# Kernel optimization log

Measured on AMD Instinct MI355X. Metric: run time of the kernel, lower is better.

The kernel has to match this reference:

```python
import jax, jax.numpy as jnp
import numpy as np

# ---- Haar DWT (levels=1, mode='zero'), matches pytorch_wavelets ordering ----
# For even H,W and filter length 2, zero-pad haar analysis reduces to
# non-overlapping 2x2 blocks. Subband order after the two 1D analyses
# (width first, then height): LL, (w-lo,h-hi), (w-hi,h-lo), HH.

def haar_dwt(x):
    a = x[..., 0::2, 0::2]
    b = x[..., 0::2, 1::2]
    c = x[..., 1::2, 0::2]
    d = x[..., 1::2, 1::2]
    ll = (a + b + c + d) * 0.5
    h0 = (a + b - c - d) * 0.5   # lo-width, hi-height
    h1 = (a - b + c - d) * 0.5   # hi-width, lo-height
    hh = (a - b - c + d) * 0.5
    return ll, jnp.stack([h0, h1, hh], axis=2)  # yh: (b,c,3,h/2,w/2)


def _interleave(u, v, axis):
    # interleave two equal-shaped arrays along `axis` (negative axis)
    s = list(u.shape)
    s[axis] *= 2
    return jnp.stack([u, v], axis=axis + len(u.shape) + 1).reshape(s)


def haar_idwt(ll, yh):
    h0, h1, hh = yh[:, :, 0], yh[:, :, 1], yh[:, :, 2]
    a = (ll + h0 + h1 + hh) * 0.5
    b = (ll + h0 - h1 - hh) * 0.5
    c = (ll - h0 + h1 - hh) * 0.5
    d = (ll - h0 - h1 + hh) * 0.5
    top = _interleave(a, b, -1)   # even rows
    bot = _interleave(c, d, -1)   # odd rows
    return _interleave(top, bot, -2)


def batched_dynamic_conv(feat, kernels, pad):
    """feat: (b,cin,h,w), kernels: (b,cout,cin,kh,kw) -> (b,cout,h,w).
    Per-sample kernels via grouped conv (batch as groups)."""
    bsz, cin, h, w = feat.shape
    cout, kh, kw = kernels.shape[1], kernels.shape[3], kernels.shape[4]
    lhs = feat.reshape(1, bsz * cin, h, w)
    rhs = kernels.reshape(bsz * cout, cin, kh, kw)
    out = jax.lax.conv_general_dilated(
        lhs, rhs, window_strides=(1, 1), padding=[(pad, pad), (pad, pad)],
        dimension_numbers=('NCHW', 'OIHW', 'NCHW'), feature_group_count=bsz)
    return out.reshape(bsz, cout, h, w)


def _dyn_conv_subband(feat, sub_kernels, attn_w, attn_b, pad=1):
    # attention: 1x1 conv -> global avg pool -> softmax over kernel_num
    logits = jnp.einsum('bchw,kc->bk', feat, attn_w) / (feat.shape[-2] * feat.shape[-1]) + attn_b
    att = jax.nn.softmax(logits, axis=1)                       # (b,K)
    kernels = jnp.einsum('bk,koiuv->boiuv', att, sub_kernels)  # (b,cout,cin,kh,kw)
    return batched_dynamic_conv(feat, kernels, pad)


def setup_inputs() -> dict:
    key = jax.random.key(0)
    k1, k2, k3, k4 = jax.random.split(key, 4)
    B, C, H, W = 8, 64, 128, 128
    K, SUB, COUT, KS = 4, 4, 64, 3  # kernel_num, 1+3*levels, out_channels, kernel_size
    return {
        'x': jax.random.normal(k1, (B, C, H, W), dtype=jnp.float32),
        'wt_kernels': jax.random.normal(k2, (K, SUB, COUT, C, KS, KS), dtype=jnp.float32) * 0.02,
        'attn_w': jax.random.normal(k3, (K, C), dtype=jnp.float32) * 0.1,
        'attn_b': jnp.zeros((K,), dtype=jnp.float32),
    }


def reference(x, wt_kernels, attn_w, attn_b):
    ll, yh = haar_dwt(x)
    subbands = [ll, yh[:, :, 0], yh[:, :, 1], yh[:, :, 2]]
    outs = [_dyn_conv_subband(sb, wt_kernels[:, i], attn_w, attn_b, pad=1)
            for i, sb in enumerate(subbands)]
    rec_yh = jnp.stack(outs[1:4], axis=2)  # (b,cout,3,h/2,w/2)
    return haar_idwt(outs[0], rec_yh)
```

## Files before the change

kernel.cpp:

```cpp
#include <hip/hip_runtime.h>
#include <hip/hip_bf16.h>
#include <math.h>


typedef __bf16 bf16x8 __attribute__((ext_vector_type(8)));
typedef float f32x4 __attribute__((ext_vector_type(4)));

__device__ __forceinline__ bf16x8 as_bf16x8(uint4 u) {
    union { uint4 a; bf16x8 b; } c; c.a = u; return c.b;
}
__device__ __forceinline__ unsigned short bf16bits(float f) {
    __hip_bfloat16 h = __float2bfloat16(f);
    union { __hip_bfloat16 h; unsigned short u; } c; c.h = h; return c.u;
}
__device__ __forceinline__ void gload_lds16(const uint4* g, uint4* l) {
    __builtin_amdgcn_global_load_lds(
        (const __attribute__((address_space(1))) unsigned int*)g,
        (__attribute__((address_space(3))) unsigned int*)l, 16, 0, 0);
}

#define FPLANE 34848
#define FROW   528

__global__ __launch_bounds__(256)
void dwt_kernel(const float* __restrict__ x, const float* __restrict__ attn_w,
                unsigned short* __restrict__ feats, float* __restrict__ plog) {
    __shared__ uint4 sT[2304];
    __shared__ float sred[64][4];
    unsigned short* sTu = (unsigned short*)sT;
    int y = blockIdx.x, b = blockIdx.y;
    int t = threadIdx.x;
    int c = t >> 2, q = t & 3;

    const float4* r0 = (const float4*)x + ((size_t)(b * 64 + c) * 128 + 2 * y) * 32;
    const float4* r1 = r0 + 32;

    float s0 = 0.f, s1 = 0.f, s2 = 0.f, s3 = 0.f;
    #pragma unroll
    for (int i = 0; i < 8; ++i) {
        int f = i * 4 + q;
        float4 p = r0[f], qq = r1[f];
        int xo = 2 * f;
        {
            float a = p.x, bb = p.y, cc = qq.x, dd = qq.y;
            float ll = (a + bb + cc + dd) * 0.5f, h0 = (a + bb - cc - dd) * 0.5f;
            float h1 = (a - bb + cc - dd) * 0.5f, hh = (a - bb - cc + dd) * 0.5f;
            s0 += ll; s1 += h0; s2 += h1; s3 += hh;
            sTu[0 * 4608 + xo * 72 + c] = bf16bits(ll);
            sTu[1 * 4608 + xo * 72 + c] = bf16bits(h0);
            sTu[2 * 4608 + xo * 72 + c] = bf16bits(h1);
            sTu[3 * 4608 + xo * 72 + c] = bf16bits(hh);
        }
        {
            float a = p.z, bb = p.w, cc = qq.z, dd = qq.w;
            float ll = (a + bb + cc + dd) * 0.5f, h0 = (a + bb - cc - dd) * 0.5f;
            float h1 = (a - bb + cc - dd) * 0.5f, hh = (a - bb - cc + dd) * 0.5f;
            s0 += ll; s1 += h0; s2 += h1; s3 += hh;
            sTu[0 * 4608 + (xo + 1) * 72 + c] = bf16bits(ll);
            sTu[1 * 4608 + (xo + 1) * 72 + c] = bf16bits(h0);
            sTu[2 * 4608 + (xo + 1) * 72 + c] = bf16bits(h1);
            sTu[3 * 4608 + (xo + 1) * 72 + c] = bf16bits(hh);
        }
    }
    s0 += __shfl_xor(s0, 1); s0 += __shfl_xor(s0, 2);
    s1 += __shfl_xor(s1, 1); s1 += __shfl_xor(s1, 2);
    s2 += __shfl_xor(s2, 1); s2 += __shfl_xor(s2, 2);
    s3 += __shfl_xor(s3, 1); s3 += __shfl_xor(s3, 2);
    if (q == 0) { sred[c][0] = s0; sred[c][1] = s1; sred[c][2] = s2; sred[c][3] = s3; }
    __syncthreads();
    if (t < 16) {
        int sub = t >> 2, k = t & 3;
        float acc = 0.f;
        #pragma unroll 8
        for (int cc = 0; cc < 64; ++cc)
            acc += attn_w[k * 64 + cc] * sred[cc][sub];
        plog[((size_t)(b * 4 + sub) * 4 + k) * 64 + y] = acc;
    }
    uint4* fpad = (uint4*)feats;
    const uint4 zz = make_uint4(0u, 0u, 0u, 0u);
    for (int e = t; e < 2112; e += 256) {
        int s = e / 528, r = e - s * 528;
        int px = r >> 3, ck = r & 7;
        uint4 v = zz;
        if (px >= 1 && px <= 64) v = sT[s * 576 + (px - 1) * 9 + ck];
        fpad[((size_t)(b * 4 + s) * 66 + (y + 1)) * FROW + r] = v;
    }
    if (y == 0) {
        for (int e = t; e < 2112; e += 256) {
            int s = e / 528, r = e - s * 528;
            fpad[(size_t)(b * 4 + s) * 66 * FROW + r] = zz;
        }
    } else if (y == 63) {
        for (int e = t; e < 2112; e += 256) {
            int s = e / 528, r = e - s * 528;
            fpad[((size_t)(b * 4 + s) * 66 + 65) * FROW + r] = zz;
        }
    }
}

__global__ __launch_bounds__(256)
void mix_kernel(const float* __restrict__ wt, const float* __restrict__ attn_b,
                const float* __restrict__ plog, unsigned short* __restrict__ wmix) {
    __shared__ float sLw[4][576];
    __shared__ float satt[8][4];
    int co = blockIdx.x, sub = blockIdx.y;
    int t = threadIdx.x;

    if (t < 32) {
        int b = t >> 2, k = t & 3;
        const float* pp = plog + ((size_t)(b * 4 + sub) * 4 + k) * 64;
        float acc = 0.f;
        #pragma unroll 8
        for (int yy = 0; yy < 64; ++yy) acc += pp[yy];
        float logit = acc * (1.0f / 4096.0f) + attn_b[k];
        float m = fmaxf(logit, __shfl_xor(logit, 1));
        m = fmaxf(m, __shfl_xor(m, 2));
        float e = expf(logit - m);
        float s = e + __shfl_xor(e, 1);
        s += __shfl_xor(s, 2);
        satt[b][k] = e / s;
    }
    for (int e = t; e < 2304; e += 256) {
        int k = e / 576, r = e - k * 576;
        sLw[k][r] = wt[((size_t)(k * 4 + sub) * 64 + co) * 576 + r];
    }
    __syncthreads();
    #pragma unroll
    for (int j = 0; j < 18; ++j) {
        int idx = j * 256 + t;
        int b = idx / 576;
        int r = idx - b * 576;
        int tap = r >> 6, ci = r & 63;
        int wi = ci * 9 + tap;
        float v = satt[b][0] * sLw[0][wi] + satt[b][1] * sLw[1][wi]
                + satt[b][2] * sLw[2][wi] + satt[b][3] * sLw[3][wi];
        wmix[((size_t)(b * 4 + sub) * 9 + tap) * 4096 + co * 64 + ci] = bf16bits(v);
    }
}

__device__ __forceinline__ void stage_phase(const uint4* __restrict__ fp,
                                            const uint4* __restrict__ wch,
                                            uint4* sAb, uint4* sWb,
                                            int y0, int x0, int cg, int ck8, int t) {
    #pragma unroll
    for (int i = 0; i < 3; ++i) {
        int e = t + i * 256;
        int py = e / 72, rr = e - py * 72, px = rr >> 2, g = rr & 3;
        gload_lds16(fp + (size_t)((y0 + py) * 66 + x0 + px) * 8 + ck8 + g, &sAb[e]);
    }
    #pragma unroll
    for (int i = 0; i < 4; ++i) {
        int e = t + i * 256;
        int tap = e >> 7, rr = e & 127, co = rr >> 2, g = rr & 3;
        gload_lds16(wch + tap * 512 + (cg * 32 + co) * 8 + ck8 + g, &sWb[e]);
    }
    if (t < 128) {
        int e = 1024 + t;
        int tap = e >> 7, rr = e & 127, co = rr >> 2, g = rr & 3;
        gload_lds16(wch + tap * 512 + (cg * 32 + co) * 8 + ck8 + g, &sWb[e]);
    }
}

__global__ __launch_bounds__(256, 2)
void conv_idwt_kernel(const unsigned short* __restrict__ feats,
                      const unsigned short* __restrict__ wmix,
                      float* __restrict__ out) {
    __shared__ uint4 sA[2][768];
    __shared__ uint4 sW[2][1152];
    int lin = blockIdx.x;
    int b = lin & 7;
    int rest = lin >> 3;
    int cg = rest >> 5, tile = rest & 31;
    int y0 = (tile >> 2) * 8, x0 = (tile & 3) * 16;
    int t = threadIdx.x, w = t >> 6, l = t & 63;
    int l16 = l & 15, kg = l >> 4;
    int wy4 = (w >> 1) * 4, wn = w & 1;

    const uint4* fpb = (const uint4*)feats + (size_t)b * 4 * FPLANE;
    const uint4* wcb = (const uint4*)wmix + (size_t)b * 4 * 4608;

    f32x4 accQ[4][4];
    f32x4 accS[4];
    #pragma unroll
    for (int qd = 0; qd < 4; ++qd)
        #pragma unroll
        for (int r = 0; r < 4; ++r)
            accQ[qd][r] = (f32x4){0.f, 0.f, 0.f, 0.f};
    #pragma unroll
    for (int r = 0; r < 4; ++r) accS[r] = (f32x4){0.f, 0.f, 0.f, 0.f};

    stage_phase(fpb, wcb, sA[0], sW[0], y0, x0, cg, 0, t);
    __syncthreads();

    #pragma unroll
    for (int p = 0; p < 8; ++p) {
        const int sub = p >> 1;
        if (p < 7) {
            const int ns = (p + 1) >> 1, nc = ((p + 1) & 1) * 4;
            stage_phase(fpb + (size_t)ns * FPLANE, wcb + (size_t)ns * 4608,
                        sA[(p + 1) & 1], sW[(p + 1) & 1], y0, x0, cg, nc, t);
        }
        {
            const uint4* A = sA[p & 1];
            const uint4* W = sW[p & 1];
            uint4 af[4][3];
            #pragma unroll
            for (int i = 0; i < 4; ++i)
                #pragma unroll
                for (int dx = 0; dx < 3; ++dx)
                    af[i][dx] = A[((wy4 + i) * 18 + l16 + dx) * 4 + kg];
            __builtin_amdgcn_s_setprio(1);
            #pragma unroll
            for (int dy = 0; dy < 3; ++dy) {
                if (dy > 0) {
                    #pragma unroll
                    for (int i = 0; i < 3; ++i)
                        #pragma unroll
                        for (int dx = 0; dx < 3; ++dx)
                            af[i][dx] = af[i + 1][dx];
                    #pragma unroll
                    for (int dx = 0; dx < 3; ++dx)
                        af[3][dx] = A[((wy4 + dy + 3) * 18 + l16 + dx) * 4 + kg];
                }
                #pragma unroll
                for (int dx = 0; dx < 3; ++dx) {
                    int tap = dy * 3 + dx;
                    bf16x8 bw = as_bf16x8(W[tap * 128 + (wn * 16 + l16) * 4 + kg]);
                    #pragma unroll
                    for (int r = 0; r < 4; ++r)
                        accS[r] = __builtin_amdgcn_mfma_f32_16x16x32_bf16(
                            as_bf16x8(af[r][dx]), bw, accS[r], 0, 0, 0);
                }
            }
            __builtin_amdgcn_s_setprio(0);
        }
        if (p & 1) {
            const float g1 = (sub <= 1) ? 1.f : -1.f;
            const float g2 = (sub == 0 || sub == 2) ? 1.f : -1.f;
            const float g3 = (sub == 0 || sub == 3) ? 1.f : -1.f;
            #pragma unroll
            for (int r = 0; r < 4; ++r) {
                #pragma unroll
                for (int j = 0; j < 4; ++j) {
                    float v = accS[r][j];
                    accQ[0][r][j] += v;
                    accQ[1][r][j] += g1 * v;
                    accQ[2][r][j] += g2 * v;
                    accQ[3][r][j] += g3 * v;
                    accS[r][j] = 0.f;
                }
            }
        }
        __syncthreads();
    }

    #pragma unroll
    for (int r = 0; r < 4; ++r) {
        int y = y0 + wy4 + r;
        int co = cg * 32 + wn * 16 + l16;
        float* otop = out + ((size_t)(b * 64 + co) * 128 + 2 * y) * 128
                          + 2 * (x0 + kg * 4);
        float* obot = otop + 128;
        #pragma unroll
        for (int jp = 0; jp < 2; ++jp) {
            float4 vt, vb;
            vt.x = 0.5f * accQ[0][r][2 * jp];
            vt.y = 0.5f * accQ[1][r][2 * jp];
            vt.z = 0.5f * accQ[0][r][2 * jp + 1];
            vt.w = 0.5f * accQ[1][r][2 * jp + 1];
            vb.x = 0.5f * accQ[2][r][2 * jp];
            vb.y = 0.5f * accQ[3][r][2 * jp];
            vb.z = 0.5f * accQ[2][r][2 * jp + 1];
            vb.w = 0.5f * accQ[3][r][2 * jp + 1];
            *(float4*)(otop + 4 * jp) = vt;
            *(float4*)(obot + 4 * jp) = vb;
        }
    }
}

extern "C" void kernel_launch(void* const* d_in, const int* in_sizes, int n_in,
                              void* d_out, int out_size, void* d_ws, size_t ws_size,
                              hipStream_t stream) {
    const float* x  = (const float*)d_in[0];
    const float* wt = (const float*)d_in[1];
    const float* aw = (const float*)d_in[2];
    const float* ab = (const float*)d_in[3];
    float* out = (float*)d_out;
    char* ws = (char*)d_ws;

    float* plog           = (float*)ws;
    unsigned short* feats = (unsigned short*)(ws + 32768);
    unsigned short* wmix  = (unsigned short*)(ws + 32768 + 17842176);

    hipLaunchKernelGGL(dwt_kernel, dim3(64, 8), dim3(256), 0, stream, x, aw, feats, plog);
    hipLaunchKernelGGL(mix_kernel, dim3(64, 4), dim3(256), 0, stream, wt, ab, plog, wmix);
    hipLaunchKernelGGL(conv_idwt_kernel, dim3(512), dim3(256), 0, stream,
                       feats, wmix, out);
}
```

Before: 117.0 us.

## Fuse DWT, kernel mixing and conv into one persistent kernel with grid barriers

Merges the three launches (DWT, attention/kernel mix, conv+IDWT) into one 512-block kernel that uses software grid barriers built on global atomics, plus a tiny init kernel that resets the barrier counters. The first feature tile is prefetched before the mix phase, so the load overlaps the weight mixing. This removes launch gaps and tail effects between stages. In exchange it depends on all 512 blocks being co-resident (2 per CU) or it can deadlock, and it adds atomic spin-wait overhead.

```diff
diff --git a/kernel.cpp b/kernel.cpp
--- a/kernel.cpp
+++ b/kernel.cpp
@@ -22,162 +22,194 @@
 #define FPLANE 34848
 #define FROW   528
 
-__global__ __launch_bounds__(256)
-void dwt_kernel(const float* __restrict__ x, const float* __restrict__ attn_w,
-                unsigned short* __restrict__ feats, float* __restrict__ plog) {
-    __shared__ uint4 sT[2304];
-    __shared__ float sred[64][4];
-    unsigned short* sTu = (unsigned short*)sT;
-    int y = blockIdx.x, b = blockIdx.y;
-    int t = threadIdx.x;
-    int c = t >> 2, q = t & 3;
-
-    const float4* r0 = (const float4*)x + ((size_t)(b * 64 + c) * 128 + 2 * y) * 32;
-    const float4* r1 = r0 + 32;
-
-    float s0 = 0.f, s1 = 0.f, s2 = 0.f, s3 = 0.f;
-    #pragma unroll
-    for (int i = 0; i < 8; ++i) {
-        int f = i * 4 + q;
-        float4 p = r0[f], qq = r1[f];
-        int xo = 2 * f;
-        {
-            float a = p.x, bb = p.y, cc = qq.x, dd = qq.y;
-            float ll = (a + bb + cc + dd) * 0.5f, h0 = (a + bb - cc - dd) * 0.5f;
-            float h1 = (a - bb + cc - dd) * 0.5f, hh = (a - bb - cc + dd) * 0.5f;
-            s0 += ll; s1 += h0; s2 += h1; s3 += hh;
-            sTu[0 * 4608 + xo * 72 + c] = bf16bits(ll);
-            sTu[1 * 4608 + xo * 72 + c] = bf16bits(h0);
-            sTu[2 * 4608 + xo * 72 + c] = bf16bits(h1);
-            sTu[3 * 4608 + xo * 72 + c] = bf16bits(hh);
-        }
-        {
-            float a = p.z, bb = p.w, cc = qq.z, dd = qq.w;
-            float ll = (a + bb + cc + dd) * 0.5f, h0 = (a + bb - cc - dd) * 0.5f;
-            float h1 = (a - bb + cc - dd) * 0.5f, hh = (a - bb - cc + dd) * 0.5f;
-            s0 += ll; s1 += h0; s2 += h1; s3 += hh;
-            sTu[0 * 4608 + (xo + 1) * 72 + c] = bf16bits(ll);
-            sTu[1 * 4608 + (xo + 1) * 72 + c] = bf16bits(h0);
-            sTu[2 * 4608 + (xo + 1) * 72 + c] = bf16bits(h1);
-            sTu[3 * 4608 + (xo + 1) * 72 + c] = bf16bits(hh);
-        }
-    }
-    s0 += __shfl_xor(s0, 1); s0 += __shfl_xor(s0, 2);
-    s1 += __shfl_xor(s1, 1); s1 += __shfl_xor(s1, 2);
-    s2 += __shfl_xor(s2, 1); s2 += __shfl_xor(s2, 2);
-    s3 += __shfl_xor(s3, 1); s3 += __shfl_xor(s3, 2);
-    if (q == 0) { sred[c][0] = s0; sred[c][1] = s1; sred[c][2] = s2; sred[c][3] = s3; }
+__device__ __forceinline__ void gbar(unsigned* ctr, unsigned* rel,
+                                     unsigned target, unsigned gen) {
     __syncthreads();
-    if (t < 16) {
-        int sub = t >> 2, k = t & 3;
-        float acc = 0.f;
-        #pragma unroll 8
-        for (int cc = 0; cc < 64; ++cc)
-            acc += attn_w[k * 64 + cc] * sred[cc][sub];
-        plog[((size_t)(b * 4 + sub) * 4 + k) * 64 + y] = acc;
-    }
-    uint4* fpad = (uint4*)feats;
-    const uint4 zz = make_uint4(0u, 0u, 0u, 0u);
-    for (int e = t; e < 2112; e += 256) {
-        int s = e / 528, r = e - s * 528;
-        int px = r >> 3, ck = r & 7;
-        uint4 v = zz;
-        if (px >= 1 && px <= 64) v = sT[s * 576 + (px - 1) * 9 + ck];
-        fpad[((size_t)(b * 4 + s) * 66 + (y + 1)) * FROW + r] = v;
-    }
-    if (y == 0) {
-        for (int e = t; e < 2112; e += 256) {
-            int s = e / 528, r = e - s * 528;
-            fpad[(size_t)(b * 4 + s) * 66 * FROW + r] = zz;
-        }
-    } else if (y == 63) {
-        for (int e = t; e < 2112; e += 256) {
-            int s = e / 528, r = e - s * 528;
-            fpad[((size_t)(b * 4 + s) * 66 + 65) * FROW + r] = zz;
-        }
-    }
-}
-
-__global__ __launch_bounds__(256)
-void mix_kernel(const float* __restrict__ wt, const float* __restrict__ attn_b,
-                const float* __restrict__ plog, unsigned short* __restrict__ wmix) {
-    __shared__ float sLw[4][576];
-    __shared__ float satt[8][4];
-    int co = blockIdx.x, sub = blockIdx.y;
-    int t = threadIdx.x;
-
-    if (t < 32) {
-        int b = t >> 2, k = t & 3;
-        const float* pp = plog + ((size_t)(b * 4 + sub) * 4 + k) * 64;
-        float acc = 0.f;
-        #pragma unroll 8
-        for (int yy = 0; yy < 64; ++yy) acc += pp[yy];
-        float logit = acc * (1.0f / 4096.0f) + attn_b[k];
-        float m = fmaxf(logit, __shfl_xor(logit, 1));
-        m = fmaxf(m, __shfl_xor(m, 2));
-        float e = expf(logit - m);
-        float s = e + __shfl_xor(e, 1);
-        s += __shfl_xor(s, 2);
-        satt[b][k] = e / s;
-    }
-    for (int e = t; e < 2304; e += 256) {
-        int k = e / 576, r = e - k * 576;
-        sLw[k][r] = wt[((size_t)(k * 4 + sub) * 64 + co) * 576 + r];
+    if (threadIdx.x == 0) {
+        __threadfence();
+        unsigned old = atomicAdd(ctr, 1u);
+        if (old == target - 1u) {
+            __hip_atomic_store(rel, gen, __ATOMIC_RELEASE,
+                               __HIP_MEMORY_SCOPE_AGENT);
+        } else {
+            while (__hip_atomic_load(rel, __ATOMIC_ACQUIRE,
+                                     __HIP_MEMORY_SCOPE_AGENT) < gen)
+                __builtin_amdgcn_s_sleep(4);
+        }
+        __threadfence();
     }
     __syncthreads();
-    #pragma unroll
-    for (int j = 0; j < 18; ++j) {
-        int idx = j * 256 + t;
-        int b = idx / 576;
-        int r = idx - b * 576;
-        int tap = r >> 6, ci = r & 63;
-        int wi = ci * 9 + tap;
-        float v = satt[b][0] * sLw[0][wi] + satt[b][1] * sLw[1][wi]
-                + satt[b][2] * sLw[2][wi] + satt[b][3] * sLw[3][wi];
-        wmix[((size_t)(b * 4 + sub) * 9 + tap) * 4096 + co * 64 + ci] = bf16bits(v);
-    }
-}
-
-__device__ __forceinline__ void stage_phase(const uint4* __restrict__ fp,
-                                            const uint4* __restrict__ wch,
-                                            uint4* sAb, uint4* sWb,
-                                            int y0, int x0, int cg, int ck8, int t) {
+}
+
+__global__ void binit_kernel(unsigned* p) {
+    __hip_atomic_store(&p[0], 0u, __ATOMIC_RELAXED, __HIP_MEMORY_SCOPE_AGENT);
+    __hip_atomic_store(&p[1], 0u, __ATOMIC_RELAXED, __HIP_MEMORY_SCOPE_AGENT);
+}
+
+__device__ __forceinline__ void stage_A(const uint4* __restrict__ fp, uint4* sAb,
+                                        int y0, int x0, int ck8, int t) {
     #pragma unroll
     for (int i = 0; i < 3; ++i) {
         int e = t + i * 256;
         int py = e / 72, rr = e - py * 72, px = rr >> 2, g = rr & 3;
         gload_lds16(fp + (size_t)((y0 + py) * 66 + x0 + px) * 8 + ck8 + g, &sAb[e]);
     }
+}
+__device__ __forceinline__ void stage_W(const uint4* __restrict__ wch, uint4* sWb,
+                                        int cgv, int ck8, int t) {
     #pragma unroll
     for (int i = 0; i < 4; ++i) {
         int e = t + i * 256;
         int tap = e >> 7, rr = e & 127, co = rr >> 2, g = rr & 3;
-        gload_lds16(wch + tap * 512 + (cg * 32 + co) * 8 + ck8 + g, &sWb[e]);
+        gload_lds16(wch + tap * 512 + (cgv * 32 + co) * 8 + ck8 + g, &sWb[e]);
     }
     if (t < 128) {
         int e = 1024 + t;
         int tap = e >> 7, rr = e & 127, co = rr >> 2, g = rr & 3;
-        gload_lds16(wch + tap * 512 + (cg * 32 + co) * 8 + ck8 + g, &sWb[e]);
+        gload_lds16(wch + tap * 512 + (cgv * 32 + co) * 8 + ck8 + g, &sWb[e]);
     }
 }
 
 __global__ __launch_bounds__(256, 2)
-void conv_idwt_kernel(const unsigned short* __restrict__ feats,
-                      const unsigned short* __restrict__ wmix,
-                      float* __restrict__ out) {
-    __shared__ uint4 sA[2][768];
-    __shared__ uint4 sW[2][1152];
-    int lin = blockIdx.x;
-    int b = lin & 7;
+void fused_kernel(const float* __restrict__ x, const float* __restrict__ wt,
+                  const float* __restrict__ attn_w, const float* __restrict__ attn_b,
+                  float* __restrict__ plog, unsigned short* __restrict__ feats,
+                  unsigned short* __restrict__ wmix, unsigned* __restrict__ bstate,
+                  float* __restrict__ out) {
+    __shared__ uint4 smem[3840];
+    int lin = blockIdx.x, t = threadIdx.x;
+    unsigned* bctr = bstate;
+    unsigned* brel = bstate + 1;
+
+    {
+        uint4* sT = smem;
+        unsigned short* sTu = (unsigned short*)smem;
+        float (*sred)[4] = (float(*)[4])((char*)smem + 36864);
+        int y = lin >> 3, b = lin & 7;
+        int c = t >> 2, q = t & 3;
+
+        const float4* r0 = (const float4*)x + ((size_t)(b * 64 + c) * 128 + 2 * y) * 32;
+        const float4* r1 = r0 + 32;
+
+        float s0 = 0.f, s1 = 0.f, s2 = 0.f, s3 = 0.f;
+        #pragma unroll
+        for (int i = 0; i < 8; ++i) {
+            int f = i * 4 + q;
+            float4 p = r0[f], qq = r1[f];
+            int xo = 2 * f;
+            {
+                float a = p.x, bb = p.y, cc = qq.x, dd = qq.y;
+                float ll = (a + bb + cc + dd) * 0.5f, h0 = (a + bb - cc - dd) * 0.5f;
+                float h1 = (a - bb + cc - dd) * 0.5f, hh = (a - bb - cc + dd) * 0.5f;
+                s0 += ll; s1 += h0; s2 += h1; s3 += hh;
+                sTu[0 * 4608 + xo * 72 + c] = bf16bits(ll);
+                sTu[1 * 4608 + xo * 72 + c] = bf16bits(h0);
+                sTu[2 * 4608 + xo * 72 + c] = bf16bits(h1);
+                sTu[3 * 4608 + xo * 72 + c] = bf16bits(hh);
+            }
+            {
+                float a = p.z, bb = p.w, cc = qq.z, dd = qq.w;
+                float ll = (a + bb + cc + dd) * 0.5f, h0 = (a + bb - cc - dd) * 0.5f;
+                float h1 = (a - bb + cc - dd) * 0.5f, hh = (a - bb - cc + dd) * 0.5f;
+                s0 += ll; s1 += h0; s2 += h1; s3 += hh;
+                sTu[0 * 4608 + (xo + 1) * 72 + c] = bf16bits(ll);
+                sTu[1 * 4608 + (xo + 1) * 72 + c] = bf16bits(h0);
+                sTu[2 * 4608 + (xo + 1) * 72 + c] = bf16bits(h1);
+                sTu[3 * 4608 + (xo + 1) * 72 + c] = bf16bits(hh);
+            }
+        }
+        s0 += __shfl_xor(s0, 1); s0 += __shfl_xor(s0, 2);
+        s1 += __shfl_xor(s1, 1); s1 += __shfl_xor(s1, 2);
+        s2 += __shfl_xor(s2, 1); s2 += __shfl_xor(s2, 2);
+        s3 += __shfl_xor(s3, 1); s3 += __shfl_xor(s3, 2);
+        if (q == 0) { sred[c][0] = s0; sred[c][1] = s1; sred[c][2] = s2; sred[c][3] = s3; }
+        __syncthreads();
+        if (t < 16) {
+            int sub = t >> 2, k = t & 3;
+            float acc = 0.f;
+            #pragma unroll 8
+            for (int cc = 0; cc < 64; ++cc)
+                acc += attn_w[k * 64 + cc] * sred[cc][sub];
+            plog[((size_t)(b * 4 + sub) * 4 + k) * 64 + y] = acc;
+        }
+        uint4* fpad = (uint4*)feats;
+        const uint4 zz = make_uint4(0u, 0u, 0u, 0u);
+        for (int e = t; e < 2112; e += 256) {
+            int s = e / 528, r = e - s * 528;
+            int px = r >> 3, ck = r & 7;
+            uint4 v = zz;
+            if (px >= 1 && px <= 64) v = sT[s * 576 + (px - 1) * 9 + ck];
+            fpad[((size_t)(b * 4 + s) * 66 + (y + 1)) * FROW + r] = v;
+        }
+        if (y == 0) {
+            for (int e = t; e < 2112; e += 256) {
+                int s = e / 528, r = e - s * 528;
+                fpad[(size_t)(b * 4 + s) * 66 * FROW + r] = zz;
+            }
+        } else if (y == 63) {
+            for (int e = t; e < 2112; e += 256) {
+                int s = e / 528, r = e - s * 528;
+                fpad[((size_t)(b * 4 + s) * 66 + 65) * FROW + r] = zz;
+            }
+        }
+    }
+    gbar(bctr, brel, 512u, 1u);
+
+    int b2 = lin & 7;
     int rest = lin >> 3;
-    int cg = rest >> 5, tile = rest & 31;
+    int cgv = rest >> 5, tile = rest & 31;
     int y0 = (tile >> 2) * 8, x0 = (tile & 3) * 16;
-    int t = threadIdx.x, w = t >> 6, l = t & 63;
+    uint4* sA = smem;
+    uint4* sW = smem + 1536;
+    const uint4* fpb = (const uint4*)feats + (size_t)b2 * 4 * FPLANE;
+    const uint4* wcb = (const uint4*)wmix + (size_t)b2 * 4 * 4608;
+
+    stage_A(fpb, sA, y0, x0, 0, t);
+
+    {
+        float* sLw = (float*)(smem + 1536);
+        float* satt = (float*)((char*)(smem + 1536) + 9216);
+        int unit = lin & 255, bb0 = (lin >> 8) * 4;
+        int co = unit & 63, sub = unit >> 6;
+        if (t < 16) {
+            int bl = t >> 2, k = t & 3, b = bb0 + bl;
+            const float* pp = plog + ((size_t)(b * 4 + sub) * 4 + k) * 64;
+            float acc = 0.f;
+            #pragma unroll 8
+            for (int yy = 0; yy < 64; ++yy) acc += pp[yy];
+            float logit = acc * (1.0f / 4096.0f) + attn_b[k];
+            float m = fmaxf(logit, __shfl_xor(logit, 1));
+            m = fmaxf(m, __shfl_xor(m, 2));
+            float e = expf(logit - m);
+            float s = e + __shfl_xor(e, 1);
+            s += __shfl_xor(s, 2);
+            satt[bl * 4 + k] = e / s;
+        }
+        for (int e = t; e < 2304; e += 256) {
+            int k = e / 576, r = e - k * 576;
+            sLw[k * 576 + r] = wt[((size_t)(k * 4 + sub) * 64 + co) * 576 + r];
+        }
+        __syncthreads();
+        #pragma unroll
+        for (int j = 0; j < 9; ++j) {
+            int idx = j * 256 + t;
+            int bl = idx / 576;
+            int r = idx - bl * 576;
+            int tap = r >> 6, ci = r & 63;
+            int wi = ci * 9 + tap;
+            float v = satt[bl * 4 + 0] * sLw[0 * 576 + wi]
+                    + satt[bl * 4 + 1] * sLw[1 * 576 + wi]
+                    + satt[bl * 4 + 2] * sLw[2 * 576 + wi]
+                    + satt[bl * 4 + 3] * sLw[3 * 576 + wi];
+            wmix[((size_t)((bb0 + bl) * 4 + sub) * 9 + tap) * 4096 + co * 64 + ci] =
+                bf16bits(v);
+        }
+    }
+    gbar(bctr, brel, 1024u, 2u);
+
+    int w = t >> 6, l = t & 63;
     int l16 = l & 15, kg = l >> 4;
     int wy4 = (w >> 1) * 4, wn = w & 1;
-
-    const uint4* fpb = (const uint4*)feats + (size_t)b * 4 * FPLANE;
-    const uint4* wcb = (const uint4*)wmix + (size_t)b * 4 * 4608;
 
     f32x4 accQ[4][4];
     f32x4 accS[4];
@@ -189,7 +221,7 @@
     #pragma unroll
     for (int r = 0; r < 4; ++r) accS[r] = (f32x4){0.f, 0.f, 0.f, 0.f};
 
-    stage_phase(fpb, wcb, sA[0], sW[0], y0, x0, cg, 0, t);
+    stage_W(wcb, sW, cgv, 0, t);
     __syncthreads();
 
     #pragma unroll
@@ -197,12 +229,12 @@
         const int sub = p >> 1;
         if (p < 7) {
             const int ns = (p + 1) >> 1, nc = ((p + 1) & 1) * 4;
-            stage_phase(fpb + (size_t)ns * FPLANE, wcb + (size_t)ns * 4608,
-                        sA[(p + 1) & 1], sW[(p + 1) & 1], y0, x0, cg, nc, t);
+            stage_A(fpb + (size_t)ns * FPLANE, sA + ((p + 1) & 1) * 768, y0, x0, nc, t);
+            stage_W(wcb + (size_t)ns * 4608, sW + ((p + 1) & 1) * 1152, cgv, nc, t);
         }
         {
-            const uint4* A = sA[p & 1];
-            const uint4* W = sW[p & 1];
+            const uint4* A = sA + (p & 1) * 768;
+            const uint4* W = sW + (p & 1) * 1152;
             uint4 af[4][3];
             #pragma unroll
             for (int i = 0; i < 4; ++i)
@@ -257,8 +289,8 @@
     #pragma unroll
     for (int r = 0; r < 4; ++r) {
         int y = y0 + wy4 + r;
-        int co = cg * 32 + wn * 16 + l16;
-        float* otop = out + ((size_t)(b * 64 + co) * 128 + 2 * y) * 128
+        int co = cgv * 32 + wn * 16 + l16;
+        float* otop = out + ((size_t)(b2 * 64 + co) * 128 + 2 * y) * 128
                           + 2 * (x0 + kg * 4);
         float* obot = otop + 128;
         #pragma unroll
@@ -291,9 +323,9 @@
     float* plog           = (float*)ws;
     unsigned short* feats = (unsigned short*)(ws + 32768);
     unsigned short* wmix  = (unsigned short*)(ws + 32768 + 17842176);
-
-    hipLaunchKernelGGL(dwt_kernel, dim3(64, 8), dim3(256), 0, stream, x, aw, feats, plog);
-    hipLaunchKernelGGL(mix_kernel, dim3(64, 4), dim3(256), 0, stream, wt, ab, plog, wmix);
-    hipLaunchKernelGGL(conv_idwt_kernel, dim3(512), dim3(256), 0, stream,
-                       feats, wmix, out);
-}
+    unsigned* bstate      = (unsigned*)(ws + 32768 + 17842176 + 2359296);
+
+    hipLaunchKernelGGL(binit_kernel, dim3(1), dim3(1), 0, stream, bstate);
+    hipLaunchKernelGGL(fused_kernel, dim3(512), dim3(256), 0, stream,
+                       x, wt, aw, ab, plog, feats, wmix, bstate, out);
+}
```

Result: slower. 228.9 us (+95.7%).

## Halve per-block output-channel tile to double grid and raise occupancy

Applied to the files above, without the earlier changes.

The conv kernel now gives each block 16 output channels instead of 32, so the grid doubles to 1024 blocks. Each wave covers 2 output rows instead of 4, and the whole 4-row input window is preloaded up front rather than slid row by row. The weight LDS buffer halves and launch bounds rise to 3 blocks per CU, aiming for more waves in flight on the 256-CU part. In exchange, each input tile is staged twice (once per channel group) and there are fewer MFMAs per LDS load.

```diff
diff --git a/kernel.cpp b/kernel.cpp
--- a/kernel.cpp
+++ b/kernel.cpp
@@ -138,58 +138,60 @@
     }
 }
 
-__device__ __forceinline__ void stage_phase(const uint4* __restrict__ fp,
-                                            const uint4* __restrict__ wch,
-                                            uint4* sAb, uint4* sWb,
-                                            int y0, int x0, int cg, int ck8, int t) {
+__device__ __forceinline__ void stage_A(const uint4* __restrict__ fp, uint4* sAb,
+                                        int y0, int x0, int ck8, int t) {
     #pragma unroll
     for (int i = 0; i < 3; ++i) {
         int e = t + i * 256;
         int py = e / 72, rr = e - py * 72, px = rr >> 2, g = rr & 3;
         gload_lds16(fp + (size_t)((y0 + py) * 66 + x0 + px) * 8 + ck8 + g, &sAb[e]);
     }
-    #pragma unroll
-    for (int i = 0; i < 4; ++i) {
+}
+__device__ __forceinline__ void stage_W(const uint4* __restrict__ wch, uint4* sWb,
+                                        int cgv, int ck8, int t) {
+    #pragma unroll
+    for (int i = 0; i < 2; ++i) {
         int e = t + i * 256;
-        int tap = e >> 7, rr = e & 127, co = rr >> 2, g = rr & 3;
-        gload_lds16(wch + tap * 512 + (cg * 32 + co) * 8 + ck8 + g, &sWb[e]);
-    }
-    if (t < 128) {
-        int e = 1024 + t;
-        int tap = e >> 7, rr = e & 127, co = rr >> 2, g = rr & 3;
-        gload_lds16(wch + tap * 512 + (cg * 32 + co) * 8 + ck8 + g, &sWb[e]);
-    }
-}
-
-__global__ __launch_bounds__(256, 2)
+        int tap = e >> 6, rr = e & 63, co = rr >> 2, g = rr & 3;
+        gload_lds16(wch + tap * 512 + (cgv * 16 + co) * 8 + ck8 + g, &sWb[e]);
+    }
+    if (t < 64) {
+        int e = 512 + t;
+        int tap = e >> 6, rr = e & 63, co = rr >> 2, g = rr & 3;
+        gload_lds16(wch + tap * 512 + (cgv * 16 + co) * 8 + ck8 + g, &sWb[e]);
+    }
+}
+
+__global__ __launch_bounds__(256, 3)
 void conv_idwt_kernel(const unsigned short* __restrict__ feats,
                       const unsigned short* __restrict__ wmix,
                       float* __restrict__ out) {
     __shared__ uint4 sA[2][768];
-    __shared__ uint4 sW[2][1152];
+    __shared__ uint4 sW[2][576];
     int lin = blockIdx.x;
     int b = lin & 7;
     int rest = lin >> 3;
-    int cg = rest >> 5, tile = rest & 31;
+    int cgv = rest >> 5, tile = rest & 31;
     int y0 = (tile >> 2) * 8, x0 = (tile & 3) * 16;
     int t = threadIdx.x, w = t >> 6, l = t & 63;
     int l16 = l & 15, kg = l >> 4;
-    int wy4 = (w >> 1) * 4, wn = w & 1;
+    int wy2 = w * 2;
 
     const uint4* fpb = (const uint4*)feats + (size_t)b * 4 * FPLANE;
     const uint4* wcb = (const uint4*)wmix + (size_t)b * 4 * 4608;
 
-    f32x4 accQ[4][4];
-    f32x4 accS[4];
+    f32x4 accQ[4][2];
+    f32x4 accS[2];
     #pragma unroll
     for (int qd = 0; qd < 4; ++qd)
         #pragma unroll
-        for (int r = 0; r < 4; ++r)
+        for (int r = 0; r < 2; ++r)
             accQ[qd][r] = (f32x4){0.f, 0.f, 0.f, 0.f};
     #pragma unroll
-    for (int r = 0; r < 4; ++r) accS[r] = (f32x4){0.f, 0.f, 0.f, 0.f};
-
-    stage_phase(fpb, wcb, sA[0], sW[0], y0, x0, cg, 0, t);
+    for (int r = 0; r < 2; ++r) accS[r] = (f32x4){0.f, 0.f, 0.f, 0.f};
+
+    stage_A(fpb, sA[0], y0, x0, 0, t);
+    stage_W(wcb, sW[0], cgv, 0, t);
     __syncthreads();
 
     #pragma unroll
@@ -197,8 +199,8 @@
         const int sub = p >> 1;
         if (p < 7) {
             const int ns = (p + 1) >> 1, nc = ((p + 1) & 1) * 4;
-            stage_phase(fpb + (size_t)ns * FPLANE, wcb + (size_t)ns * 4608,
-                        sA[(p + 1) & 1], sW[(p + 1) & 1], y0, x0, cg, nc, t);
+            stage_A(fpb + (size_t)ns * FPLANE, sA[(p + 1) & 1], y0, x0, nc, t);
+            stage_W(wcb + (size_t)ns * 4608, sW[(p + 1) & 1], cgv, nc, t);
         }
         {
             const uint4* A = sA[p & 1];
@@ -208,28 +210,18 @@
             for (int i = 0; i < 4; ++i)
                 #pragma unroll
                 for (int dx = 0; dx < 3; ++dx)
-                    af[i][dx] = A[((wy4 + i) * 18 + l16 + dx) * 4 + kg];
+                    af[i][dx] = A[((wy2 + i) * 18 + l16 + dx) * 4 + kg];
             __builtin_amdgcn_s_setprio(1);
             #pragma unroll
             for (int dy = 0; dy < 3; ++dy) {
-                if (dy > 0) {
-                    #pragma unroll
-                    for (int i = 0; i < 3; ++i)
-                        #pragma unroll
-                        for (int dx = 0; dx < 3; ++dx)
-                            af[i][dx] = af[i + 1][dx];
-                    #pragma unroll
-                    for (int dx = 0; dx < 3; ++dx)
-                        af[3][dx] = A[((wy4 + dy + 3) * 18 + l16 + dx) * 4 + kg];
-                }
                 #pragma unroll
                 for (int dx = 0; dx < 3; ++dx) {
                     int tap = dy * 3 + dx;
-                    bf16x8 bw = as_bf16x8(W[tap * 128 + (wn * 16 + l16) * 4 + kg]);
+                    bf16x8 bw = as_bf16x8(W[tap * 64 + l16 * 4 + kg]);
                     #pragma unroll
-                    for (int r = 0; r < 4; ++r)
+                    for (int r = 0; r < 2; ++r)
                         accS[r] = __builtin_amdgcn_mfma_f32_16x16x32_bf16(
-                            as_bf16x8(af[r][dx]), bw, accS[r], 0, 0, 0);
+                            as_bf16x8(af[dy + r][dx]), bw, accS[r], 0, 0, 0);
                 }
             }
             __builtin_amdgcn_s_setprio(0);
@@ -239,7 +231,7 @@
             const float g2 = (sub == 0 || sub == 2) ? 1.f : -1.f;
             const float g3 = (sub == 0 || sub == 3) ? 1.f : -1.f;
             #pragma unroll
-            for (int r = 0; r < 4; ++r) {
+            for (int r = 0; r < 2; ++r) {
                 #pragma unroll
                 for (int j = 0; j < 4; ++j) {
                     float v = accS[r][j];
@@ -255,9 +247,9 @@
     }
 
     #pragma unroll
-    for (int r = 0; r < 4; ++r) {
-        int y = y0 + wy4 + r;
-        int co = cg * 32 + wn * 16 + l16;
+    for (int r = 0; r < 2; ++r) {
+        int y = y0 + wy2 + r;
+        int co = cgv * 16 + l16;
         float* otop = out + ((size_t)(b * 64 + co) * 128 + 2 * y) * 128
                           + 2 * (x0 + kg * 4);
         float* obot = otop + 128;
@@ -294,6 +286,6 @@
 
     hipLaunchKernelGGL(dwt_kernel, dim3(64, 8), dim3(256), 0, stream, x, aw, feats, plog);
     hipLaunchKernelGGL(mix_kernel, dim3(64, 4), dim3(256), 0, stream, wt, ab, plog, wmix);
-    hipLaunchKernelGGL(conv_idwt_kernel, dim3(512), dim3(256), 0, stream,
+    hipLaunchKernelGGL(conv_idwt_kernel, dim3(1024), dim3(256), 0, stream,
                        feats, wmix, out);
 }
```

Result: slower. 123.7 us (+5.8%).
